# Kernel optimization log

Measured on AMD Instinct MI355X. Metric: run time of the kernel, lower is better.

## Reference

```python
import jax, jax.numpy as jnp
import numpy as np

NUM_HEADS = 16

def setup_inputs() -> dict:
    key = jax.random.key(0)
    k1, k2, k3 = jax.random.split(key, 3)
    B, S, D = 2, 2048, 1024
    x = jax.random.normal(k1, (B, S, D), dtype=jnp.float32)
    Wqkv = jax.random.normal(k2, (D, 3 * D), dtype=jnp.float32) * (1.0 / np.sqrt(D))
    bqkv = jnp.zeros((3 * D,), dtype=jnp.float32)
    Wo = jax.random.normal(k3, (D, D), dtype=jnp.float32) * (1.0 / np.sqrt(D))
    bo = jnp.zeros((D,), dtype=jnp.float32)
    return {"x": x, "Wqkv": Wqkv, "bqkv": bqkv, "Wo": Wo, "bo": bo}

def reference(x, Wqkv, bqkv, Wo, bo):
    B, S, D = x.shape
    H = NUM_HEADS
    hd = D // H
    # qkv projection, split into per-head q, k, v: [B, H, S, hd]
    qkv = (x @ Wqkv + bqkv).reshape(B, S, H, 3 * hd).transpose(0, 2, 1, 3)
    q, k, v = jnp.split(qkv, 3, axis=-1)
    # causal attention scores [B, H, S, S]
    scores = jnp.einsum('bhqd,bhkd->bhqk', q, k)
    causal = jnp.tril(jnp.ones((S, S), dtype=bool))  # True = keep
    scores = jnp.where(causal, scores, -jnp.inf)
    attn = jax.nn.softmax(scores / np.sqrt(hd).astype(np.float32), axis=-1)
    # dropout is identity in eval mode
    ctx = jnp.einsum('bhqk,bhkd->bhqd', attn, v)  # [B, H, S, hd]
    ctx = ctx.transpose(0, 2, 1, 3).reshape(B, S, D)
    return ctx @ Wo + bo
```

## Files before the change

### kernel.cpp

```cpp
#include <hip/hip_runtime.h>


typedef __attribute__((ext_vector_type(8))) __bf16 bf16x8;
typedef __attribute__((ext_vector_type(4))) float f32x4;
typedef __attribute__((ext_vector_type(4))) short short4v;

__device__ __forceinline__ unsigned short f2bf(float f) {
    union { float f; unsigned u; } v; v.f = f;
    unsigned r = v.u + 0x7fffu + ((v.u >> 16) & 1u);
    return (unsigned short)(r >> 16);
}

__device__ __forceinline__ float bf2f(unsigned short u) {
    return __builtin_bit_cast(float, (unsigned)u << 16);
}

__device__ __forceinline__ unsigned pack_bf16x2_trunc(float a, float b) {
#if defined(__HIP_DEVICE_COMPILE__)
    return __builtin_amdgcn_perm(__builtin_bit_cast(unsigned, a),
                                 __builtin_bit_cast(unsigned, b), 0x03020706u);
#else
    return 0u;
#endif
}

__device__ __forceinline__ float fast_exp2(float x) {
#if defined(__HIP_DEVICE_COMPILE__)
    return __builtin_amdgcn_exp2f(x);
#else
    return x;
#endif
}

__device__ __forceinline__ void async_copy16(const unsigned short* g, unsigned short* l) {
    __builtin_amdgcn_global_load_lds(
        (const __attribute__((address_space(1))) unsigned int*)g,
        (__attribute__((address_space(3))) unsigned int*)l, 16, 0, 0);
}

__device__ __forceinline__ f32x4 mfma16x16x16(short4v a, short4v b, f32x4 c) {
#if defined(__HIP_DEVICE_COMPILE__)
    return __builtin_amdgcn_mfma_f32_16x16x16bf16_1k(a, b, c, 0, 0, 0);
#else
    return c;
#endif
}

__device__ __forceinline__ void convert_body(
    const float* __restrict__ in, unsigned short* __restrict__ out, int blk)
{
    size_t i = ((size_t)blk * 256 + threadIdx.x) * 8;
    float4 v0 = *(const float4*)(in + i);
    float4 v1 = *(const float4*)(in + i + 4);
    ushort4 a, b;
    a.x = f2bf(v0.x); a.y = f2bf(v0.y); a.z = f2bf(v0.z); a.w = f2bf(v0.w);
    b.x = f2bf(v1.x); b.y = f2bf(v1.y); b.z = f2bf(v1.z); b.w = f2bf(v1.w);
    *(ushort4*)(out + i) = a;
    *(ushort4*)(out + i + 4) = b;
}

__device__ __forceinline__ void transpose_body(
    const float* __restrict__ in, unsigned short* __restrict__ out,
    int K, int N, int bx, int by, float T[64][65])
{
    const int tid = threadIdx.x;
    const int n0 = bx * 64, k0 = by * 64;
#pragma unroll
    for (int i = 0; i < 4; i++) {
        int idx = tid + i * 256;
        int r = idx >> 4, c4 = (idx & 15) * 4;
        float4 v = *(const float4*)(in + (size_t)(k0 + r) * N + n0 + c4);
        T[r][c4 + 0] = v.x; T[r][c4 + 1] = v.y; T[r][c4 + 2] = v.z; T[r][c4 + 3] = v.w;
    }
    __syncthreads();
#pragma unroll
    for (int i = 0; i < 4; i++) {
        int idx = tid + i * 256;
        int n = idx >> 4, k4 = (idx & 15) * 4;
        ushort4 o;
        o.x = f2bf(T[k4 + 0][n]); o.y = f2bf(T[k4 + 1][n]);
        o.z = f2bf(T[k4 + 2][n]); o.w = f2bf(T[k4 + 3][n]);
        *(ushort4*)(out + (size_t)(n0 + n) * K + k0 + k4) = o;
    }
}

__global__ __launch_bounds__(256) void prep(
    const float* __restrict__ x, const float* __restrict__ Wqkv, const float* __restrict__ Wo,
    unsigned short* __restrict__ xbf, unsigned short* __restrict__ wqkvT,
    unsigned short* __restrict__ woT)
{
    __shared__ float T[64][65];
    const int i = blockIdx.x;
    if (i < 2048) {
        convert_body(x, xbf, i);
    } else if (i < 2048 + 768) {
        int j = i - 2048;
        transpose_body(Wqkv, wqkvT, 1024, 3072, j % 48, j / 48, T);
    } else {
        int j = i - 2816;
        transpose_body(Wo, woT, 1024, 1024, j % 16, j / 16, T);
    }
}

__global__ __launch_bounds__(256) void convert_f32_bf16(
    const float* __restrict__ in, unsigned short* __restrict__ out)
{
    convert_body(in, out, blockIdx.x);
}

__global__ __launch_bounds__(256) void transpose_f32_bf16(
    const float* __restrict__ in, unsigned short* __restrict__ out, int K, int N)
{
    __shared__ float T[64][65];
    transpose_body(in, out, K, N, blockIdx.x, blockIdx.y, T);
}

__global__ __launch_bounds__(256) void transpose_v(
    const unsigned short* __restrict__ vrow, unsigned short* __restrict__ vt)
{
    __shared__ unsigned short T[64 * 72];
    const int tid = threadIdx.x;
    const int bh = blockIdx.y;
    const int s0 = blockIdx.x * 64;
    const unsigned short* src = vrow + ((size_t)bh * 2048 + s0) * 64;
    unsigned short* dst = vt + (size_t)bh * 64 * 2048 + s0;
#pragma unroll
    for (int i = 0; i < 2; i++) {
        int idx = tid + i * 256;
        int s = idx >> 3, dg = (idx & 7) * 8;
        *(uint4*)&T[s * 72 + dg] = *(const uint4*)(src + s * 64 + dg);
    }
    __syncthreads();
#pragma unroll
    for (int i = 0; i < 2; i++) {
        int idx = tid + i * 256;
        int d = idx >> 3, sg = (idx & 7) * 8;
        ushort4 a, b;
        a.x = T[(sg + 0) * 72 + d]; a.y = T[(sg + 1) * 72 + d];
        a.z = T[(sg + 2) * 72 + d]; a.w = T[(sg + 3) * 72 + d];
        b.x = T[(sg + 4) * 72 + d]; b.y = T[(sg + 5) * 72 + d];
        b.z = T[(sg + 6) * 72 + d]; b.w = T[(sg + 7) * 72 + d];
        *(ushort4*)(dst + (size_t)d * 2048 + sg) = a;
        *(ushort4*)(dst + (size_t)d * 2048 + sg + 4) = b;
    }
}

__global__ __launch_bounds__(256) void gemm_qkv_bf(
    const unsigned short* __restrict__ Xbf,
    const unsigned short* __restrict__ WT,
    const float* __restrict__ bias,
    unsigned short* __restrict__ qws, unsigned short* __restrict__ kws,
    unsigned short* __restrict__ vrow)
{
    const int K = 1024;
    __shared__ __align__(16) unsigned short smem[128 * 136];
    unsigned short* As = smem;
    unsigned short* Bs = smem + 8192;
    const int tid = threadIdx.x;
    const int m0 = blockIdx.y * 128, n0 = blockIdx.x * 128;
    const int wave = tid >> 6, lane = tid & 63;
    const int wm = (wave >> 1) * 64, wn = (wave & 1) * 64;
    const int quad = lane >> 4, l16 = lane & 15;
    const int lrow = lane >> 3, lgrp = lane & 7;
    const int sg = lgrp ^ lrow;

    f32x4 acc[4][4];
    const f32x4 Z4 = {0.f, 0.f, 0.f, 0.f};
#pragma unroll
    for (int i = 0; i < 4; i++)
#pragma unroll
        for (int j = 0; j < 4; j++) acc[i][j] = Z4;

    for (int k0 = 0; k0 < K; k0 += 64) {
        __syncthreads();
#pragma unroll
        for (int c = 0; c < 4; c++) {
            int nb = (wave * 4 + c) * 8;
            async_copy16(Xbf + (size_t)(m0 + nb + lrow) * K + k0 + sg * 8, &As[nb * 64]);
            async_copy16(WT  + (size_t)(n0 + nb + lrow) * K + k0 + sg * 8, &Bs[nb * 64]);
        }
        __syncthreads();
#pragma unroll
        for (int kk = 0; kk < 2; kk++) {
            int pg = ((kk * 4 + quad) ^ (l16 & 7)) * 8;
            bf16x8 af[4], bfr[4];
#pragma unroll
            for (int mi = 0; mi < 4; mi++) af[mi] = *(const bf16x8*)&As[(wm + mi * 16 + l16) * 64 + pg];
#pragma unroll
            for (int ni = 0; ni < 4; ni++) bfr[ni] = *(const bf16x8*)&Bs[(wn + ni * 16 + l16) * 64 + pg];
#pragma unroll
            for (int mi = 0; mi < 4; mi++)
#pragma unroll
                for (int ni = 0; ni < 4; ni++)
                    acc[mi][ni] = __builtin_amdgcn_mfma_f32_16x16x32_bf16(af[mi], bfr[ni], acc[mi][ni], 0, 0, 0);
        }
    }
    __syncthreads();
#pragma unroll
    for (int ni = 0; ni < 4; ni++) {
        int colL = wn + ni * 16 + l16;
        int col = n0 + colL;
        int t = (col % 192) >> 6;
        float bv = bias[col];
        float scl = (t == 1) ? 0.18033688f : 1.0f;
#pragma unroll
        for (int mi = 0; mi < 4; mi++)
#pragma unroll
            for (int r = 0; r < 4; r++) {
                int row = wm + mi * 16 + quad * 4 + r;
                smem[row * 136 + colL] = f2bf((acc[mi][ni][r] + bv) * scl);
            }
    }
    __syncthreads();
#pragma unroll
    for (int i = 0; i < 8; i++) {
        int idx = tid + i * 256;
        int row = idx >> 4, g = idx & 15;
        int colL = g * 8;
        uint4 w = *(const uint4*)&smem[row * 136 + colL];
        int col = n0 + colL;
        int h = col / 192, rem = col % 192, t = rem >> 6, d = rem & 63;
        int grow = m0 + row;
        int b = grow >> 11, s = grow & 2047;
        unsigned short* dst = (t == 0) ? qws : (t == 1) ? kws : vrow;
        *(uint4*)(dst + ((size_t)(b * 16 + h) * 2048 + s) * 64 + d) = w;
    }
}

#define J(t, s, e, c) ((unsigned)(t) | ((unsigned)(s) << 8) | ((unsigned)(e) << 16) | ((unsigned)(c) << 24))
__device__ __constant__ unsigned ATTN_JOBS[60] = {
    J(22,0,12,0), J(23,0,12,0), J(23,12,24,1), J(11,0,12,0),
    J(20,0,11,0), J(21,0,11,0), J(21,11,22,1), J(22,12,23,1),
    J(30,0,11,0), J(31,0,11,0), J(31,11,22,1), J(10,0,11,0),
    J(18,0,10,0), J(19,0,10,0), J(19,10,20,1), J(20,11,21,1),
    J(27,0,10,0), J(28,0,10,0), J(28,10,20,1), J(29,0,10,0),
    J(29,10,20,1), J(29,20,30,2), J(30,11,21,1), J(30,21,31,2),
    J(31,22,32,2), J(9,0,10,0),
    J(16,0,9,0), J(17,0,9,0), J(17,9,18,1), J(18,10,19,1),
    J(24,0,9,0), J(25,0,9,0), J(25,9,18,1), J(26,0,9,0),
    J(26,9,18,1), J(26,18,27,2), J(27,10,19,1), J(27,19,28,2),
    J(28,20,29,2), J(8,0,9,0),
    J(14,0,8,0), J(15,0,8,0), J(15,8,16,1), J(16,9,17,1),
    J(24,9,17,1), J(24,17,25,2), J(25,18,26,2), J(7,0,8,0),
    J(12,0,7,0), J(13,0,7,0), J(13,7,14,1), J(14,8,15,1), J(6,0,7,0),
    J(12,7,13,1), J(5,0,6,0), J(4,0,5,0), J(3,0,4,0), J(2,0,3,0),
    J(1,0,2,0), J(0,0,1,0),
};
#undef J

__global__ __launch_bounds__(128) void attn(
    const unsigned short* __restrict__ qws, const unsigned short* __restrict__ kws,
    const unsigned short* __restrict__ vtws, unsigned short* __restrict__ ctx,
    unsigned short* __restrict__ Opart, float* __restrict__ lpart)
{
    __shared__ __align__(16) unsigned short Qs[64 * 64];
    __shared__ __align__(16) unsigned short Ks[64 * 64];
    __shared__ __align__(16) unsigned short Vt[64][72];

    const int tid = threadIdx.x;
    const int wave = tid >> 6, lane = tid & 63, quad = lane >> 4, l16 = lane & 15;
    const int lrow = lane >> 3, lgrp = lane & 7;
    const int sg = lgrp ^ lrow;

    const unsigned job = ATTN_JOBS[blockIdx.x >> 5];
    const int bh = blockIdx.x & 31;
    const int tile = job & 0xff;
    const int js = (job >> 8) & 0xff, je = (job >> 16) & 0xff;
    const int chunk = (job >> 24) & 0xff;
    const int q0 = tile * 64;
    const bool split = tile >= 12;

    const unsigned short* Q  = qws + (size_t)bh * 2048 * 64;
    const unsigned short* Kp = kws + (size_t)bh * 2048 * 64;
    const unsigned short* Vp = vtws + (size_t)bh * 64 * 2048;

#pragma unroll
    for (int c = 0; c < 4; c++) {
        int rb = (wave * 4 + c) * 8;
        async_copy16(Q + (size_t)(q0 + rb + lrow) * 64 + sg * 8, &Qs[rb * 64]);
    }

    const int wq = wave * 32;
    f32x4 o[4][2];
    const f32x4 Z4 = {0.f, 0.f, 0.f, 0.f};
#pragma unroll
    for (int dt = 0; dt < 4; dt++)
#pragma unroll
        for (int qt = 0; qt < 2; qt++) o[dt][qt] = Z4;
    float lsum[2] = {0.f, 0.f};

    for (int j = js; j < je; j++) {
        const int kb0 = j * 64;
        __syncthreads();
#pragma unroll
        for (int c = 0; c < 4; c++) {
            int rb = (wave * 4 + c) * 8;
            async_copy16(Kp + (size_t)(kb0 + rb + lrow) * 64 + sg * 8, &Ks[rb * 64]);
        }
#pragma unroll
        for (int ii = 0; ii < 4; ii++) {
            int id2 = tid + ii * 128;
            int row = id2 >> 3, c = (id2 & 7) * 8;
            *(uint4*)&Vt[row][c] = *(const uint4*)(Vp + (size_t)row * 2048 + kb0 + c);
        }
        __syncthreads();

        if (kb0 <= q0 + wq + 31) {
            f32x4 sc[4][2];
#pragma unroll
            for (int kt = 0; kt < 4; kt++)
#pragma unroll
                for (int qt = 0; qt < 2; qt++) sc[kt][qt] = Z4;
#pragma unroll
            for (int kk = 0; kk < 2; kk++) {
                int pg = ((kk * 4 + quad) ^ (l16 & 7)) * 8;
                bf16x8 ak[4], bq[2];
#pragma unroll
                for (int kt = 0; kt < 4; kt++) ak[kt] = *(const bf16x8*)&Ks[(kt * 16 + l16) * 64 + pg];
#pragma unroll
                for (int qt = 0; qt < 2; qt++) bq[qt] = *(const bf16x8*)&Qs[(wq + qt * 16 + l16) * 64 + pg];
#pragma unroll
                for (int kt = 0; kt < 4; kt++)
#pragma unroll
                    for (int qt = 0; qt < 2; qt++)
                        sc[kt][qt] = __builtin_amdgcn_mfma_f32_16x16x32_bf16(ak[kt], bq[qt], sc[kt][qt], 0, 0, 0);
            }
            short4v pb[4][2];
            if (kb0 + 63 <= q0 + wq) {
#pragma unroll
                for (int qt = 0; qt < 2; qt++)
#pragma unroll
                    for (int kt = 0; kt < 4; kt++) {
                        float p0 = fast_exp2(sc[kt][qt][0]);
                        float p1 = fast_exp2(sc[kt][qt][1]);
                        float p2 = fast_exp2(sc[kt][qt][2]);
                        float p3 = fast_exp2(sc[kt][qt][3]);
                        lsum[qt] += (p0 + p1) + (p2 + p3);
                        uint2 uu;
                        uu.x = pack_bf16x2_trunc(p0, p1);
                        uu.y = pack_bf16x2_trunc(p2, p3);
                        pb[kt][qt] = __builtin_bit_cast(short4v, uu);
                    }
            } else {
#pragma unroll
                for (int qt = 0; qt < 2; qt++) {
                    int qg = q0 + wq + qt * 16 + l16;
#pragma unroll
                    for (int kt = 0; kt < 4; kt++) {
                        float p[4];
#pragma unroll
                        for (int r = 0; r < 4; r++) {
                            int key = kb0 + kt * 16 + quad * 4 + r;
                            float t = fast_exp2(sc[kt][qt][r]);
                            p[r] = (key <= qg) ? t : 0.f;
                        }
                        lsum[qt] += (p[0] + p[1]) + (p[2] + p[3]);
                        uint2 uu;
                        uu.x = pack_bf16x2_trunc(p[0], p[1]);
                        uu.y = pack_bf16x2_trunc(p[2], p[3]);
                        pb[kt][qt] = __builtin_bit_cast(short4v, uu);
                    }
                }
            }
#pragma unroll
            for (int kt = 0; kt < 4; kt++) {
#pragma unroll
                for (int dt = 0; dt < 4; dt++) {
                    short4v av = *(const short4v*)&Vt[dt * 16 + l16][kt * 16 + quad * 4];
#pragma unroll
                    for (int qt = 0; qt < 2; qt++)
                        o[dt][qt] = mfma16x16x16(av, pb[kt][qt], o[dt][qt]);
                }
            }
        }
    }
#pragma unroll
    for (int qt = 0; qt < 2; qt++) {
        lsum[qt] += __shfl_xor(lsum[qt], 16);
        lsum[qt] += __shfl_xor(lsum[qt], 32);
    }
    const int b = bh >> 4, h = bh & 15;
    if (!split) {
#pragma unroll
        for (int qt = 0; qt < 2; qt++) {
            int qg = q0 + wq + qt * 16 + l16;
            float inv = 1.0f / lsum[qt];
#pragma unroll
            for (int dt = 0; dt < 4; dt++) {
                ushort4 ov;
                ov.x = f2bf(o[dt][qt][0] * inv);
                ov.y = f2bf(o[dt][qt][1] * inv);
                ov.z = f2bf(o[dt][qt][2] * inv);
                ov.w = f2bf(o[dt][qt][3] * inv);
                *(ushort4*)(ctx + (size_t)(b * 2048 + qg) * 1024 + h * 64 + dt * 16 + quad * 4) = ov;
            }
        }
    } else {
        const int ls = (tile < 24) ? (tile - 12) * 2 + chunk
                                   : 24 + (tile - 24) * 3 + chunk;
        float* lp = lpart + ((size_t)bh * 48 + ls) * 64;
#pragma unroll
        for (int qt = 0; qt < 2; qt++) {
            int rl = wq + qt * 16 + l16;
            if (quad == 0) lp[rl] = lsum[qt];
        }
        if (chunk == 0) {
#pragma unroll
            for (int qt = 0; qt < 2; qt++) {
                int qg = q0 + wq + qt * 16 + l16;
#pragma unroll
                for (int dt = 0; dt < 4; dt++) {
                    ushort4 ov;
                    ov.x = f2bf(o[dt][qt][0]);
                    ov.y = f2bf(o[dt][qt][1]);
                    ov.z = f2bf(o[dt][qt][2]);
                    ov.w = f2bf(o[dt][qt][3]);
                    *(ushort4*)(ctx + (size_t)(b * 2048 + qg) * 1024 + h * 64 + dt * 16 + quad * 4) = ov;
                }
            }
        } else {
            const int os = (tile < 24) ? (tile - 12)
                                       : 12 + (tile - 24) * 2 + (chunk - 1);
            unsigned short* ob = Opart + ((size_t)bh * 28 + os) * 4096;
#pragma unroll
            for (int qt = 0; qt < 2; qt++) {
                int rl = wq + qt * 16 + l16;
#pragma unroll
                for (int dt = 0; dt < 4; dt++) {
                    ushort4 ov;
                    ov.x = f2bf(o[dt][qt][0]);
                    ov.y = f2bf(o[dt][qt][1]);
                    ov.z = f2bf(o[dt][qt][2]);
                    ov.w = f2bf(o[dt][qt][3]);
                    *(ushort4*)(ob + (size_t)rl * 64 + dt * 16 + quad * 4) = ov;
                }
            }
        }
    }
}

__global__ __launch_bounds__(256) void attn_combine(
    const unsigned short* __restrict__ Opart, const float* __restrict__ lpart,
    unsigned short* __restrict__ ctx)
{
    const int t = 12 + blockIdx.x;
    const int bh = blockIdx.y;
    const int tid = threadIdx.x;
    const int row = tid >> 2, dg = (tid & 3) * 16;
    const int nch = (t < 24) ? 2 : 3;
    const int ls0 = (t < 24) ? (t - 12) * 2 : 24 + (t - 24) * 3;
    const float* lp = lpart + ((size_t)bh * 48 + ls0) * 64 + row;
    float lsum = lp[0] + lp[64];
    if (nch == 3) lsum += lp[128];
    const float inv = 1.0f / lsum;
    const int os0 = (t < 24) ? (t - 12) : 12 + (t - 24) * 2;
    const unsigned short* p1 = Opart + ((size_t)bh * 28 + os0) * 4096 + (size_t)row * 64 + dg;
    const int b = bh >> 4, h = bh & 15;
    unsigned short* dst = ctx + ((size_t)(b * 2048 + t * 64 + row)) * 1024 + h * 64 + dg;
#pragma unroll
    for (int g = 0; g < 2; g++) {
        ushort a0[8], a1[8], a2[8], ov[8];
        *(uint4*)a0 = *(const uint4*)(dst + g * 8);
        *(uint4*)a1 = *(const uint4*)(p1 + g * 8);
        if (nch == 3) *(uint4*)a2 = *(const uint4*)(p1 + 4096 + g * 8);
#pragma unroll
        for (int e = 0; e < 8; e++) {
            float f = bf2f(a0[e]) + bf2f(a1[e]);
            if (nch == 3) f += bf2f(a2[e]);
            ov[e] = f2bf(f * inv);
        }
        *(uint4*)(dst + g * 8) = *(const uint4*)ov;
    }
}

__global__ __launch_bounds__(256) void gemm_out(
    const unsigned short* __restrict__ Ctx, const unsigned short* __restrict__ WT,
    const float* __restrict__ bias, float* __restrict__ Out)
{
    const int K = 1024, N = 1024;
    __shared__ __align__(16) unsigned short As[64 * 64];
    __shared__ __align__(16) unsigned short Bs[128 * 64];
    const int tid = threadIdx.x;
    const int m0 = blockIdx.y * 64, n0 = blockIdx.x * 128;
    const int wave = tid >> 6, lane = tid & 63;
    const int wm = (wave >> 1) * 32, wn = (wave & 1) * 64;
    const int quad = lane >> 4, l16 = lane & 15;
    const int lrow = lane >> 3, lgrp = lane & 7;
    const int sg = lgrp ^ lrow;

    f32x4 acc[2][4];
    const f32x4 Z4 = {0.f, 0.f, 0.f, 0.f};
#pragma unroll
    for (int i = 0; i < 2; i++)
#pragma unroll
        for (int j = 0; j < 4; j++) acc[i][j] = Z4;

    for (int k0 = 0; k0 < K; k0 += 64) {
        __syncthreads();
#pragma unroll
        for (int c = 0; c < 2; c++) {
            int nb = (wave * 2 + c) * 8;
            async_copy16(Ctx + (size_t)(m0 + nb + lrow) * K + k0 + sg * 8, &As[nb * 64]);
        }
#pragma unroll
        for (int c = 0; c < 4; c++) {
            int nb = (wave * 4 + c) * 8;
            async_copy16(WT + (size_t)(n0 + nb + lrow) * K + k0 + sg * 8, &Bs[nb * 64]);
        }
        __syncthreads();
#pragma unroll
        for (int kk = 0; kk < 2; kk++) {
            int pg = ((kk * 4 + quad) ^ (l16 & 7)) * 8;
            bf16x8 af[2], bfr[4];
#pragma unroll
            for (int mi = 0; mi < 2; mi++) af[mi] = *(const bf16x8*)&As[(wm + mi * 16 + l16) * 64 + pg];
#pragma unroll
            for (int ni = 0; ni < 4; ni++) bfr[ni] = *(const bf16x8*)&Bs[(wn + ni * 16 + l16) * 64 + pg];
#pragma unroll
            for (int mi = 0; mi < 2; mi++)
#pragma unroll
                for (int ni = 0; ni < 4; ni++)
                    acc[mi][ni] = __builtin_amdgcn_mfma_f32_16x16x32_bf16(af[mi], bfr[ni], acc[mi][ni], 0, 0, 0);
        }
    }
#pragma unroll
    for (int mi = 0; mi < 2; mi++)
#pragma unroll
        for (int ni = 0; ni < 4; ni++) {
            int col = n0 + wn + ni * 16 + l16;
            float bv = bias[col];
#pragma unroll
            for (int r = 0; r < 4; r++) {
                int row = m0 + wm + mi * 16 + quad * 4 + r;
                Out[(size_t)row * N + col] = acc[mi][ni][r] + bv;
            }
        }
}

extern "C" void kernel_launch(void* const* d_in, const int* in_sizes, int n_in,
                              void* d_out, int out_size, void* d_ws, size_t ws_size,
                              hipStream_t stream) {
    const float* x    = (const float*)d_in[0];
    const float* Wqkv = (const float*)d_in[1];
    const float* bqkv = (const float*)d_in[2];
    const float* Wo   = (const float*)d_in[3];
    const float* bo   = (const float*)d_in[4];
    float* out = (float*)d_out;

    const size_t R = 4194304;
    unsigned short* q    = (unsigned short*)d_ws;
    unsigned short* k    = q + R;
    unsigned short* vrow = k + R;
    unsigned short* ctx  = vrow + R;
    unsigned short* xbf  = ctx + R;
    unsigned short* vt   = xbf;
    unsigned short* wqkvT = ctx;
    unsigned short* Opart = vrow;
    float* lpart = (float*)(vrow + (size_t)896 * 4096);

    if (ws_size >= 2 * (5 * R + 1048576)) {
        unsigned short* woT5 = q + 5 * R;
        prep<<<dim3(3072), 256, 0, stream>>>(x, Wqkv, Wo, xbf, wqkvT, woT5);
        gemm_qkv_bf<<<dim3(24, 32), 256, 0, stream>>>(xbf, wqkvT, bqkv, q, k, vrow);
        transpose_v<<<dim3(32, 32), 256, 0, stream>>>(vrow, vt);
        attn<<<dim3(1920), 128, 0, stream>>>(q, k, vt, ctx, Opart, lpart);
        attn_combine<<<dim3(20, 32), 256, 0, stream>>>(Opart, lpart, ctx);
        gemm_out<<<dim3(8, 64), 256, 0, stream>>>(ctx, woT5, bo, out);
    } else {
        unsigned short* woT = q;
        convert_f32_bf16<<<dim3(2048), 256, 0, stream>>>(x, xbf);
        transpose_f32_bf16<<<dim3(48, 16), 256, 0, stream>>>(Wqkv, wqkvT, 1024, 3072);
        gemm_qkv_bf<<<dim3(24, 32), 256, 0, stream>>>(xbf, wqkvT, bqkv, q, k, vrow);
        transpose_v<<<dim3(32, 32), 256, 0, stream>>>(vrow, vt);
        attn<<<dim3(1920), 128, 0, stream>>>(q, k, vt, ctx, Opart, lpart);
        attn_combine<<<dim3(20, 32), 256, 0, stream>>>(Opart, lpart, ctx);
        transpose_f32_bf16<<<dim3(16, 16), 256, 0, stream>>>(Wo, woT, 1024, 1024);
        gemm_out<<<dim3(8, 64), 256, 0, stream>>>(ctx, woT, bo, out);
    }
}
```

Before: 190.2 us.

## Fuse V transpose into QKV GEMM epilogue and combine split-K attention in-kernel

The QKV GEMM epilogue now writes V directly in transposed layout through an extra shared-memory tile, which removes the separate transpose_v kernel and its round trip through global memory. The attention kernel now merges split-key partial results itself: the last chunk to finish for a tile, detected with an atomic counter, performs the combine, so the attn_combine launch goes away. This adds a memset launch, threadfences and atomics, and extra shared memory in the GEMM that may reduce occupancy.

After: 331.2 us. 1.74x slower.

```diff
diff --git a/kernel.cpp b/kernel.cpp
--- a/kernel.cpp
+++ b/kernel.cpp
@@ -115,49 +115,21 @@
     transpose_body(in, out, K, N, blockIdx.x, blockIdx.y, T);
 }
 
-__global__ __launch_bounds__(256) void transpose_v(
-    const unsigned short* __restrict__ vrow, unsigned short* __restrict__ vt)
-{
-    __shared__ unsigned short T[64 * 72];
-    const int tid = threadIdx.x;
-    const int bh = blockIdx.y;
-    const int s0 = blockIdx.x * 64;
-    const unsigned short* src = vrow + ((size_t)bh * 2048 + s0) * 64;
-    unsigned short* dst = vt + (size_t)bh * 64 * 2048 + s0;
-#pragma unroll
-    for (int i = 0; i < 2; i++) {
-        int idx = tid + i * 256;
-        int s = idx >> 3, dg = (idx & 7) * 8;
-        *(uint4*)&T[s * 72 + dg] = *(const uint4*)(src + s * 64 + dg);
-    }
-    __syncthreads();
-#pragma unroll
-    for (int i = 0; i < 2; i++) {
-        int idx = tid + i * 256;
-        int d = idx >> 3, sg = (idx & 7) * 8;
-        ushort4 a, b;
-        a.x = T[(sg + 0) * 72 + d]; a.y = T[(sg + 1) * 72 + d];
-        a.z = T[(sg + 2) * 72 + d]; a.w = T[(sg + 3) * 72 + d];
-        b.x = T[(sg + 4) * 72 + d]; b.y = T[(sg + 5) * 72 + d];
-        b.z = T[(sg + 6) * 72 + d]; b.w = T[(sg + 7) * 72 + d];
-        *(ushort4*)(dst + (size_t)d * 2048 + sg) = a;
-        *(ushort4*)(dst + (size_t)d * 2048 + sg + 4) = b;
-    }
-}
-
 __global__ __launch_bounds__(256) void gemm_qkv_bf(
     const unsigned short* __restrict__ Xbf,
     const unsigned short* __restrict__ WT,
     const float* __restrict__ bias,
     unsigned short* __restrict__ qws, unsigned short* __restrict__ kws,
-    unsigned short* __restrict__ vrow)
+    unsigned short* __restrict__ vt)
 {
     const int K = 1024;
     __shared__ __align__(16) unsigned short smem[128 * 136];
+    __shared__ __align__(16) unsigned short Tv[64 * 146];
     unsigned short* As = smem;
     unsigned short* Bs = smem + 8192;
     const int tid = threadIdx.x;
     const int m0 = blockIdx.y * 128, n0 = blockIdx.x * 128;
+    const int phase = blockIdx.x % 3;
     const int wave = tid >> 6, lane = tid & 63;
     const int wm = (wave >> 1) * 64, wn = (wave & 1) * 64;
     const int quad = lane >> 4, l16 = lane & 15;
@@ -200,30 +172,68 @@
     for (int ni = 0; ni < 4; ni++) {
         int colL = wn + ni * 16 + l16;
         int col = n0 + colL;
-        int t = (col % 192) >> 6;
+        int rem = col % 192, t = rem >> 6;
         float bv = bias[col];
-        float scl = (t == 1) ? 0.18033688f : 1.0f;
-#pragma unroll
-        for (int mi = 0; mi < 4; mi++)
-#pragma unroll
-            for (int r = 0; r < 4; r++) {
-                int row = wm + mi * 16 + quad * 4 + r;
-                smem[row * 136 + colL] = f2bf((acc[mi][ni][r] + bv) * scl);
-            }
+        if (t == 2) {
+#pragma unroll
+            for (int mi = 0; mi < 4; mi++)
+#pragma unroll
+                for (int r = 0; r < 4; r++) {
+                    int row = wm + mi * 16 + quad * 4 + r;
+                    Tv[(colL & 63) * 146 + row] = f2bf(acc[mi][ni][r] + bv);
+                }
+        } else {
+            float scl = (t == 1) ? 0.18033688f : 1.0f;
+#pragma unroll
+            for (int mi = 0; mi < 4; mi++)
+#pragma unroll
+                for (int r = 0; r < 4; r++) {
+                    int row = wm + mi * 16 + quad * 4 + r;
+                    smem[row * 136 + colL] = f2bf((acc[mi][ni][r] + bv) * scl);
+                }
+        }
     }
     __syncthreads();
-#pragma unroll
-    for (int i = 0; i < 8; i++) {
-        int idx = tid + i * 256;
-        int row = idx >> 4, g = idx & 15;
-        int colL = g * 8;
-        uint4 w = *(const uint4*)&smem[row * 136 + colL];
-        int col = n0 + colL;
-        int h = col / 192, rem = col % 192, t = rem >> 6, d = rem & 63;
-        int grow = m0 + row;
-        int b = grow >> 11, s = grow & 2047;
-        unsigned short* dst = (t == 0) ? qws : (t == 1) ? kws : vrow;
-        *(uint4*)(dst + ((size_t)(b * 16 + h) * 2048 + s) * 64 + d) = w;
+    if (phase == 0) {
+#pragma unroll
+        for (int i = 0; i < 8; i++) {
+            int idx = tid + i * 256;
+            int row = idx >> 4, g = idx & 15;
+            int colL = g * 8;
+            uint4 w = *(const uint4*)&smem[row * 136 + colL];
+            int col = n0 + colL;
+            int h = col / 192, rem = col % 192, t = rem >> 6, d = rem & 63;
+            int grow = m0 + row;
+            int b = grow >> 11, s = grow & 2047;
+            unsigned short* dst = (t == 0) ? qws : kws;
+            *(uint4*)(dst + ((size_t)(b * 16 + h) * 2048 + s) * 64 + d) = w;
+        }
+    } else {
+        const int qkb = (phase == 1) ? 64 : 0;
+#pragma unroll
+        for (int i = 0; i < 4; i++) {
+            int idx = tid + i * 256;
+            int row = idx >> 3, g = idx & 7;
+            int colL = qkb + g * 8;
+            uint4 w = *(const uint4*)&smem[row * 136 + colL];
+            int col = n0 + colL;
+            int h = col / 192, rem = col % 192, t = rem >> 6, d = rem & 63;
+            int grow = m0 + row;
+            int b = grow >> 11, s = grow & 2047;
+            unsigned short* dst = (t == 0) ? qws : kws;
+            *(uint4*)(dst + ((size_t)(b * 16 + h) * 2048 + s) * 64 + d) = w;
+        }
+        const int vbase = (phase == 1) ? 0 : 64;
+        const int hv = (n0 + vbase) / 192;
+        const int bb = m0 >> 11, s0 = m0 & 2047;
+        unsigned short* vtb = vt + ((size_t)(bb * 16 + hv) * 64) * 2048 + s0;
+#pragma unroll
+        for (int i = 0; i < 4; i++) {
+            int idx = tid + i * 256;
+            int d = idx >> 4, rg = idx & 15;
+            uint4 w = *(const uint4*)&Tv[d * 146 + rg * 8];
+            *(uint4*)(vtb + (size_t)d * 2048 + rg * 8) = w;
+        }
     }
 }
 
@@ -251,11 +261,12 @@
 __global__ __launch_bounds__(128) void attn(
     const unsigned short* __restrict__ qws, const unsigned short* __restrict__ kws,
     const unsigned short* __restrict__ vtws, unsigned short* __restrict__ ctx,
-    unsigned short* __restrict__ Opart, float* __restrict__ lpart)
+    unsigned short* __restrict__ Opart, float* __restrict__ lpart, int* __restrict__ cnt)
 {
     __shared__ __align__(16) unsigned short Qs[64 * 64];
     __shared__ __align__(16) unsigned short Ks[64 * 64];
     __shared__ __align__(16) unsigned short Vt[64][72];
+    __shared__ int s_old;
 
     const int tid = threadIdx.x;
     const int wave = tid >> 6, lane = tid & 63, quad = lane >> 4, l16 = lane & 15;
@@ -395,81 +406,77 @@
                 *(ushort4*)(ctx + (size_t)(b * 2048 + qg) * 1024 + h * 64 + dt * 16 + quad * 4) = ov;
             }
         }
+        return;
+    }
+    const int nch = (tile < 24) ? 2 : 3;
+    const int ls0 = (tile < 24) ? (tile - 12) * 2 : 24 + (tile - 24) * 3;
+    const int os0 = (tile < 24) ? (tile - 12) : 12 + (tile - 24) * 2;
+    const int ls = ls0 + chunk;
+    float* lp0 = lpart + ((size_t)bh * 48 + ls) * 64;
+#pragma unroll
+    for (int qt = 0; qt < 2; qt++) {
+        int rl = wq + qt * 16 + l16;
+        if (quad == 0) lp0[rl] = lsum[qt];
+    }
+    if (chunk == 0) {
+#pragma unroll
+        for (int qt = 0; qt < 2; qt++) {
+            int qg = q0 + wq + qt * 16 + l16;
+#pragma unroll
+            for (int dt = 0; dt < 4; dt++) {
+                ushort4 ov;
+                ov.x = f2bf(o[dt][qt][0]);
+                ov.y = f2bf(o[dt][qt][1]);
+                ov.z = f2bf(o[dt][qt][2]);
+                ov.w = f2bf(o[dt][qt][3]);
+                *(ushort4*)(ctx + (size_t)(b * 2048 + qg) * 1024 + h * 64 + dt * 16 + quad * 4) = ov;
+            }
+        }
     } else {
-        const int ls = (tile < 24) ? (tile - 12) * 2 + chunk
-                                   : 24 + (tile - 24) * 3 + chunk;
-        float* lp = lpart + ((size_t)bh * 48 + ls) * 64;
+        unsigned short* ob = Opart + ((size_t)bh * 28 + os0 + (chunk - 1)) * 4096;
 #pragma unroll
         for (int qt = 0; qt < 2; qt++) {
             int rl = wq + qt * 16 + l16;
-            if (quad == 0) lp[rl] = lsum[qt];
-        }
-        if (chunk == 0) {
-#pragma unroll
-            for (int qt = 0; qt < 2; qt++) {
-                int qg = q0 + wq + qt * 16 + l16;
-#pragma unroll
-                for (int dt = 0; dt < 4; dt++) {
-                    ushort4 ov;
-                    ov.x = f2bf(o[dt][qt][0]);
-                    ov.y = f2bf(o[dt][qt][1]);
-                    ov.z = f2bf(o[dt][qt][2]);
-                    ov.w = f2bf(o[dt][qt][3]);
-                    *(ushort4*)(ctx + (size_t)(b * 2048 + qg) * 1024 + h * 64 + dt * 16 + quad * 4) = ov;
-                }
-            }
-        } else {
-            const int os = (tile < 24) ? (tile - 12)
-                                       : 12 + (tile - 24) * 2 + (chunk - 1);
-            unsigned short* ob = Opart + ((size_t)bh * 28 + os) * 4096;
-#pragma unroll
-            for (int qt = 0; qt < 2; qt++) {
-                int rl = wq + qt * 16 + l16;
-#pragma unroll
-                for (int dt = 0; dt < 4; dt++) {
-                    ushort4 ov;
-                    ov.x = f2bf(o[dt][qt][0]);
-                    ov.y = f2bf(o[dt][qt][1]);
-                    ov.z = f2bf(o[dt][qt][2]);
-                    ov.w = f2bf(o[dt][qt][3]);
-                    *(ushort4*)(ob + (size_t)rl * 64 + dt * 16 + quad * 4) = ov;
-                }
-            }
-        }
-    }
-}
-
-__global__ __launch_bounds__(256) void attn_combine(
-    const unsigned short* __restrict__ Opart, const float* __restrict__ lpart,
-    unsigned short* __restrict__ ctx)
-{
-    const int t = 12 + blockIdx.x;
-    const int bh = blockIdx.y;
-    const int tid = threadIdx.x;
-    const int row = tid >> 2, dg = (tid & 3) * 16;
-    const int nch = (t < 24) ? 2 : 3;
-    const int ls0 = (t < 24) ? (t - 12) * 2 : 24 + (t - 24) * 3;
-    const float* lp = lpart + ((size_t)bh * 48 + ls0) * 64 + row;
-    float lsum = lp[0] + lp[64];
-    if (nch == 3) lsum += lp[128];
-    const float inv = 1.0f / lsum;
-    const int os0 = (t < 24) ? (t - 12) : 12 + (t - 24) * 2;
-    const unsigned short* p1 = Opart + ((size_t)bh * 28 + os0) * 4096 + (size_t)row * 64 + dg;
-    const int b = bh >> 4, h = bh & 15;
-    unsigned short* dst = ctx + ((size_t)(b * 2048 + t * 64 + row)) * 1024 + h * 64 + dg;
-#pragma unroll
-    for (int g = 0; g < 2; g++) {
-        ushort a0[8], a1[8], a2[8], ov[8];
-        *(uint4*)a0 = *(const uint4*)(dst + g * 8);
-        *(uint4*)a1 = *(const uint4*)(p1 + g * 8);
-        if (nch == 3) *(uint4*)a2 = *(const uint4*)(p1 + 4096 + g * 8);
-#pragma unroll
-        for (int e = 0; e < 8; e++) {
-            float f = bf2f(a0[e]) + bf2f(a1[e]);
-            if (nch == 3) f += bf2f(a2[e]);
-            ov[e] = f2bf(f * inv);
-        }
-        *(uint4*)(dst + g * 8) = *(const uint4*)ov;
+#pragma unroll
+            for (int dt = 0; dt < 4; dt++) {
+                ushort4 ov;
+                ov.x = f2bf(o[dt][qt][0]);
+                ov.y = f2bf(o[dt][qt][1]);
+                ov.z = f2bf(o[dt][qt][2]);
+                ov.w = f2bf(o[dt][qt][3]);
+                *(ushort4*)(ob + (size_t)rl * 64 + dt * 16 + quad * 4) = ov;
+            }
+        }
+    }
+    __threadfence();
+    __syncthreads();
+    if (tid == 0) s_old = atomicAdd(&cnt[bh * 20 + (tile - 12)], 1);
+    __syncthreads();
+    if (s_old == nch - 1) {
+        __threadfence();
+        const float* lp = lpart + ((size_t)bh * 48 + ls0) * 64;
+        const unsigned short* pb1 = Opart + ((size_t)bh * 28 + os0) * 4096;
+        unsigned short* cbase = ctx + ((size_t)(b * 2048 + tile * 64)) * 1024 + h * 64;
+#pragma unroll
+        for (int it = 0; it < 4; it++) {
+            int idx = tid + it * 128;
+            int row = idx >> 3, g = (idx & 7) * 8;
+            float ls2 = lp[row] + lp[64 + row];
+            if (nch == 3) ls2 += lp[128 + row];
+            float inv = 1.0f / ls2;
+            unsigned short* dst = cbase + (size_t)row * 1024 + g;
+            ushort a0[8], a1[8], a2[8], ov[8];
+            *(uint4*)a0 = *(const uint4*)dst;
+            *(uint4*)a1 = *(const uint4*)(pb1 + (size_t)row * 64 + g);
+            if (nch == 3) *(uint4*)a2 = *(const uint4*)(pb1 + 4096 + (size_t)row * 64 + g);
+#pragma unroll
+            for (int e = 0; e < 8; e++) {
+                float f = bf2f(a0[e]) + bf2f(a1[e]);
+                if (nch == 3) f += bf2f(a2[e]);
+                ov[e] = f2bf(f * inv);
+            }
+            *(uint4*)dst = *(const uint4*)ov;
+        }
     }
 }
 
@@ -550,30 +557,28 @@
     const size_t R = 4194304;
     unsigned short* q    = (unsigned short*)d_ws;
     unsigned short* k    = q + R;
-    unsigned short* vrow = k + R;
-    unsigned short* ctx  = vrow + R;
+    unsigned short* vt   = k + R;
+    unsigned short* ctx  = vt + R;
     unsigned short* xbf  = ctx + R;
-    unsigned short* vt   = xbf;
     unsigned short* wqkvT = ctx;
-    unsigned short* Opart = vrow;
-    float* lpart = (float*)(vrow + (size_t)896 * 4096);
+    unsigned short* Opart = xbf;
+    float* lpart = (float*)(xbf + (size_t)896 * 4096);
+    int* cnt = (int*)(xbf + (size_t)896 * 4096 + 196608);
 
     if (ws_size >= 2 * (5 * R + 1048576)) {
         unsigned short* woT5 = q + 5 * R;
         prep<<<dim3(3072), 256, 0, stream>>>(x, Wqkv, Wo, xbf, wqkvT, woT5);
-        gemm_qkv_bf<<<dim3(24, 32), 256, 0, stream>>>(xbf, wqkvT, bqkv, q, k, vrow);
-        transpose_v<<<dim3(32, 32), 256, 0, stream>>>(vrow, vt);
-        attn<<<dim3(1920), 128, 0, stream>>>(q, k, vt, ctx, Opart, lpart);
-        attn_combine<<<dim3(20, 32), 256, 0, stream>>>(Opart, lpart, ctx);
+        gemm_qkv_bf<<<dim3(24, 32), 256, 0, stream>>>(xbf, wqkvT, bqkv, q, k, vt);
+        hipMemsetAsync(cnt, 0, 640 * sizeof(int), stream);
+        attn<<<dim3(1920), 128, 0, stream>>>(q, k, vt, ctx, Opart, lpart, cnt);
         gemm_out<<<dim3(8, 64), 256, 0, stream>>>(ctx, woT5, bo, out);
     } else {
         unsigned short* woT = q;
         convert_f32_bf16<<<dim3(2048), 256, 0, stream>>>(x, xbf);
         transpose_f32_bf16<<<dim3(48, 16), 256, 0, stream>>>(Wqkv, wqkvT, 1024, 3072);
-        gemm_qkv_bf<<<dim3(24, 32), 256, 0, stream>>>(xbf, wqkvT, bqkv, q, k, vrow);
-        transpose_v<<<dim3(32, 32), 256, 0, stream>>>(vrow, vt);
-        attn<<<dim3(1920), 128, 0, stream>>>(q, k, vt, ctx, Opart, lpart);
-        attn_combine<<<dim3(20, 32), 256, 0, stream>>>(Opart, lpart, ctx);
+        gemm_qkv_bf<<<dim3(24, 32), 256, 0, stream>>>(xbf, wqkvT, bqkv, q, k, vt);
+        hipMemsetAsync(cnt, 0, 640 * sizeof(int), stream);
+        attn<<<dim3(1920), 128, 0, stream>>>(q, k, vt, ctx, Opart, lpart, cnt);
         transpose_f32_bf16<<<dim3(16, 16), 256, 0, stream>>>(Wo, woT, 1024, 1024);
         gemm_out<<<dim3(8, 64), 256, 0, stream>>>(ctx, woT, bo, out);
     }
```
